# Kernel optimization log

Measured on AMD Instinct MI355X. Metric: run time of the kernel, lower is better.

The kernel has to match this reference:

```python
import jax, jax.numpy as jnp
import numpy as np

SINKHORN_ALPHA = 20.0
WEIGHT_LOSS_ECR = 100.0
OT_MAX_ITER = 100
STOP_THR = 0.005
EPS = 1e-16


def setup_inputs() -> dict:
    key = jax.random.key(0)
    # cost matrix: topics x vocab, nonnegative
    M = jax.random.uniform(key, (2000, 20000), dtype=jnp.float32)
    return {"M": M}


def reference(M):
    n, m = M.shape
    a = jnp.full((n, 1), 1.0 / n, dtype=M.dtype)  # uniform row marginal
    b = jnp.full((m, 1), 1.0 / m, dtype=M.dtype)  # uniform col marginal
    K = jnp.exp(-M * SINKHORN_ALPHA)              # Gibbs kernel, (n, m)

    u0 = jnp.full((n, 1), 1.0 / n, dtype=M.dtype)
    v0 = jnp.zeros((m, 1), dtype=M.dtype)
    err0 = jnp.asarray(1.0, dtype=M.dtype)
    cpt0 = jnp.asarray(0, dtype=jnp.int32)

    def cond(carry):
        u, v, err, cpt = carry
        return (err > STOP_THR) & (cpt < OT_MAX_ITER)

    def body(carry):
        u, v, err, cpt = carry
        v = b / (K.T @ u + EPS)          # (m, 1)
        u = a / (K @ v + EPS)            # (n, 1)
        cpt = cpt + 1
        # convergence check every 50 iterations (cpt % 50 == 1), as in torch
        bb = v * (K.T @ u)               # (m, 1) implied col marginal
        err_new = jnp.max(jnp.sum(jnp.abs(bb - b), axis=0))
        err = jnp.where(cpt % 50 == 1, err_new.astype(err.dtype), err)
        return (u, v, err, cpt)

    u, v, err, cpt = jax.lax.while_loop(cond, body, (u0, v0, err0, cpt0))

    transp = u * (K * v.T)               # transport plan, (n, m)
    loss_ECR = jnp.sum(transp * M)
    return loss_ECR * WEIGHT_LOSS_ECR
```

## Files before the change

### kernel.cpp

```cpp
#include <hip/hip_runtime.h>

typedef unsigned int uint32;
typedef unsigned long long uint64;
typedef float floatx2 __attribute__((ext_vector_type(2)));

#define ROWS_R 2000
#define COLS_R 20000
#define NBLK   256
#define NTHR   1024
#define NWAVE  16
#define CPB    80
#define CSTR   501
#define KDW    (CPB*CSTR)
#define KGUARD 16
#define USLOTS 101

static constexpr float A_MARG = 1.0f / 2000.0f;
static constexpr float B_MARG = 1.0f / 20000.0f;
static constexpr float EPSV   = 1e-16f;
static constexpr float THR    = 0.005f;
static constexpr float NALPHA = -20.0f;

__device__ __forceinline__ void st_dev_f32(float* p, float v) {
    __hip_atomic_store(p, v, __ATOMIC_RELAXED, __HIP_MEMORY_SCOPE_AGENT);
}
__device__ __forceinline__ float ld_dev_f32(const float* p) {
    return __hip_atomic_load(const_cast<float*>(p), __ATOMIC_RELAXED, __HIP_MEMORY_SCOPE_AGENT);
}
__device__ __forceinline__ void st_dev_f32x2(float* p, float x, float y) {
    union { float2 f; uint64 q; } u; u.f = make_float2(x, y);
    __hip_atomic_store(reinterpret_cast<uint64*>(p), u.q, __ATOMIC_RELAXED, __HIP_MEMORY_SCOPE_AGENT);
}
__device__ __forceinline__ float2 ld_dev_f32x2(const float* p) {
    union { float2 f; uint64 q; } u;
    u.q = __hip_atomic_load(reinterpret_cast<uint64*>(const_cast<float*>(p)),
                            __ATOMIC_RELAXED, __HIP_MEMORY_SCOPE_AGENT);
    return u.f;
}

__device__ __forceinline__ float halfpair_sum(float x) {
#if __has_builtin(__builtin_amdgcn_permlane32_swap)
    int xi = __float_as_int(x);
    auto sw = __builtin_amdgcn_permlane32_swap(xi, xi, false, false);
    return __int_as_float(sw[0]) + __int_as_float(sw[1]);
#else
    return x + __shfl_xor(x, 32, 64);
#endif
}

__device__ __forceinline__ void grid_barrier(uint32* ctrl, uint32 rnd) {
    asm volatile("s_waitcnt vmcnt(0)" ::: "memory");
    __syncthreads();
    if (threadIdx.x == 0) {
        const int gid = (int)(blockIdx.x >> 5);
        uint32* gcnt = ctrl + 128 + gid * 64;
        uint32* ggen = ctrl + 768 + gid * 64;
        uint32 a = __hip_atomic_fetch_add(gcnt, 1u, __ATOMIC_RELAXED, __HIP_MEMORY_SCOPE_AGENT);
        if (a == rnd * 32u + 31u) {
            uint32 r = __hip_atomic_fetch_add(ctrl, 1u, __ATOMIC_RELAXED, __HIP_MEMORY_SCOPE_AGENT);
            if (r == rnd * 8u + 7u) {
#pragma unroll
                for (int g = 0; g < 8; ++g)
                    __hip_atomic_store(ctrl + 768 + g * 64, rnd + 1u,
                                       __ATOMIC_RELAXED, __HIP_MEMORY_SCOPE_AGENT);
            }
        }
        while (__hip_atomic_load(ggen, __ATOMIC_RELAXED, __HIP_MEMORY_SCOPE_AGENT) < rnd + 1u)
            __builtin_amdgcn_s_sleep(1);
    }
    __syncthreads();
}

__global__ __launch_bounds__(256) void init_kernel(float* __restrict__ u_rot,
                                                   uint32* __restrict__ ctrl,
                                                   float* __restrict__ err2,
                                                   float* __restrict__ loss) {
    int idx = blockIdx.x * 256 + threadIdx.x;
    if (idx < 1280) ctrl[idx] = 0u;
    if (idx == 0) { err2[0] = 0.f; err2[1] = 0.f; *loss = 0.f; }
    if (idx < 2048) u_rot[idx] = (idx < ROWS_R) ? A_MARG : 0.0f;
}

__global__ __launch_bounds__(NTHR, 1) void sinkhorn_lds(
    const float* __restrict__ M,
    float* __restrict__ u_rot,
    float* __restrict__ P,
    uint32* __restrict__ ctrl,
    float* __restrict__ err2,
    float* __restrict__ loss,
    float* __restrict__ out) {
    __shared__ uint32 sK[KDW + KGUARD];
    __shared__ float  s_vloc[CPB];
    __shared__ float  s_vprev[CPB];
    __shared__ float  s_red[NWAVE * 8];
    __shared__ int    s_flag;

    const int tid  = threadIdx.x;
    const int lane = tid & 63;
    const int wav  = tid >> 6;
    const int b    = blockIdx.x;
    const int j0   = b * CPB;
    uint32 bar = 0;

    for (int i = tid; i < KDW + KGUARD; i += NTHR) sK[i] = 0u;
    __syncthreads();
    for (int q = wav; q < 500; q += NWAVE) {
#pragma unroll
        for (int ph = 0; ph < 2; ++ph) {
            const int cl = ph * 64 + lane;
            const int j  = j0 + cl;
            if ((ph == 0 || lane < 16) && j < COLS_R) {
                const float* mp = M + (size_t)(4 * q) * COLS_R + j;
                float k0 = __expf(NALPHA * mp[0]);
                float k1 = __expf(NALPHA * mp[COLS_R]);
                float k2 = __expf(NALPHA * mp[2 * COLS_R]);
                float k3 = __expf(NALPHA * mp[3 * COLS_R]);
                int lo = __builtin_amdgcn_cvt_pk_fp8_f32(k0, k1, 0, false);
                int hi = __builtin_amdgcn_cvt_pk_fp8_f32(k2, k3, lo, true);
                sK[cl * CSTR + q] = (uint32)hi;
            }
        }
    }
    __syncthreads();

    int usel = 0;

    for (int t = 1; t <= 100; ++t) {
        const bool chk  = (t == 2) || (t == 52);
        const int  slot = (t == 52) ? 1 : 0;

        const float4* u4 = reinterpret_cast<const float4*>(u_rot + (size_t)usel * 2048);
        float4 u_r[8];
#pragma unroll
        for (int s = 0; s < 8; ++s) u_r[s] = u4[s * 64 + lane];

        float e = 0.f;
#pragma unroll
        for (int q = 0; q < 5; ++q) {
            const int jl = wav * 5 + q;
            float acc = 0.f;
#pragma unroll
            for (int s = 0; s < 8; ++s) {
                uint32 kw = sK[jl * CSTR + s * 64 + lane];
                floatx2 f01 = __builtin_amdgcn_cvt_pk_f32_fp8(kw, false);
                floatx2 f23 = __builtin_amdgcn_cvt_pk_f32_fp8(kw, true);
                acc += f01.x * u_r[s].x + f01.y * u_r[s].y + f23.x * u_r[s].z + f23.y * u_r[s].w;
            }
            acc = halfpair_sum(acc);
#pragma unroll
            for (int o = 16; o; o >>= 1) acc += __shfl_xor(acc, o, 64);
            if (lane == 0) {
                float vnew = B_MARG / (acc + EPSV);
                if (chk) {
                    float vold = s_vloc[jl];
                    s_vprev[jl] = vold;
                    if (j0 + jl < COLS_R) e += fabsf(vold * acc - B_MARG);
                }
                s_vloc[jl] = vnew;
            }
        }
        if (chk && lane == 0) s_red[wav] = e;
        __syncthreads();

        float4 pa = make_float4(0.f, 0.f, 0.f, 0.f);
#pragma unroll 8
        for (int jp = 0; jp < 40; ++jp) {
            const int cl = 2 * jp + (lane >> 5);
            const int m  = lane & 31;
            uint32 kw = sK[cl * CSTR + wav * 32 + m];
            float  vv = s_vloc[cl];
            floatx2 f01 = __builtin_amdgcn_cvt_pk_f32_fp8(kw, false);
            floatx2 f23 = __builtin_amdgcn_cvt_pk_f32_fp8(kw, true);
            pa.x += f01.x * vv; pa.y += f01.y * vv;
            pa.z += f23.x * vv; pa.w += f23.y * vv;
        }
        pa.x = halfpair_sum(pa.x);
        pa.y = halfpair_sum(pa.y);
        pa.z = halfpair_sum(pa.z);
        pa.w = halfpair_sum(pa.w);
        if (lane < 32) {
            float* dst = P + (size_t)b * 2048 + wav * 128 + 4 * lane;
            st_dev_f32x2(dst,     pa.x, pa.y);
            st_dev_f32x2(dst + 2, pa.z, pa.w);
        }

        if (chk && tid == 0) {
            float s = 0.f;
            for (int k = 0; k < NWAVE; ++k) s += s_red[k];
            if (s != 0.f) atomicAdd(&err2[slot], s);
        }
        grid_barrier(ctrl, bar++);

        if (chk) {
            if (tid == 0) s_flag = (ld_dev_f32(&err2[slot]) <= THR) ? 1 : 0;
            __syncthreads();
            if (s_flag) {
                if (tid < CPB) s_vloc[tid] = s_vprev[tid];
                __syncthreads();
                break;
            }
        }

        {
            float v0 = ld_dev_f32(P + (size_t)(tid >> 3) * 2048 + 8 * b + (tid & 7));
            float v1 = ld_dev_f32(P + (size_t)((tid >> 3) + 128) * 2048 + 8 * b + (tid & 7));
            float s = v0 + v1;
            s += __shfl_xor(s, 8, 64);
            s += __shfl_xor(s, 16, 64);
            s = halfpair_sum(s);
            if (lane < 8) s_red[wav * 8 + lane] = s;
        }
        __syncthreads();
        if (tid < 8) {
            float s = 0.f;
            for (int w = 0; w < NWAVE; ++w) s += s_red[w * 8 + tid];
            const int row = 8 * b + tid;
            float val = (row < ROWS_R) ? A_MARG / (s + EPSV) : 0.0f;
            st_dev_f32(u_rot + (size_t)t * 2048 + row, val);
        }
        usel = t;
        grid_barrier(ctrl, bar++);
    }

    {
        const float* uf = u_rot + (size_t)usel * 2048;
        float acc = 0.f;
        for (int r = wav; r < ROWS_R; r += NWAVE) {
            const float uu = uf[r];
            const float* mp = M + (size_t)r * COLS_R + j0;
#pragma unroll
            for (int ph = 0; ph < 2; ++ph) {
                const int cl = ph * 64 + lane;
                if ((ph == 0 || lane < 16) && (j0 + cl) < COLS_R) {
                    float m = mp[cl];
                    acc += uu * __expf(NALPHA * m) * s_vloc[cl] * m;
                }
            }
        }
        acc = halfpair_sum(acc);
#pragma unroll
        for (int o = 16; o; o >>= 1) acc += __shfl_xor(acc, o, 64);
        if (lane == 0) s_red[wav] = acc;
        __syncthreads();
        if (tid == 0) {
            float s = 0.f;
            for (int k = 0; k < NWAVE; ++k) s += s_red[k];
            if (s != 0.f) atomicAdd(loss, s);
        }
    }
    grid_barrier(ctrl, bar++);
    if (b == 0 && tid == 0) out[0] = ld_dev_f32(loss) * 100.0f;
}


__device__ __forceinline__ float block_reduce_sum256(float v) {
#pragma unroll
    for (int o = 32; o; o >>= 1) v += __shfl_down(v, o, 64);
    __shared__ float smem[4];
    int lane = threadIdx.x & 63, w = threadIdx.x >> 6;
    if (lane == 0) smem[w] = v;
    __syncthreads();
    v = (threadIdx.x < 4) ? smem[threadIdx.x] : 0.0f;
    v += __shfl_down(v, 2, 64);
    v += __shfl_down(v, 1, 64);
    return v;
}

__global__ __launch_bounds__(256) void fb_init(float* u, float* vden, int* done, float* err, float* loss) {
    int idx = blockIdx.x * 256 + threadIdx.x;
    if (idx == 0) { *done = 0; *err = 0.0f; *loss = 0.0f; }
    if (idx < ROWS_R) u[idx] = A_MARG;
    if (idx < COLS_R) vden[idx] = 0.0f;
}
__global__ __launch_bounds__(256) void fb_colpass(const float* __restrict__ M, const float* __restrict__ u,
                                                  float* __restrict__ vden, const int* __restrict__ done) {
    if (*done) return;
    int c4 = blockIdx.x * 256 + threadIdx.x;
    if (c4 >= 5000) return;
    int r0 = blockIdx.y * 50;
    float4 acc = make_float4(0.f, 0.f, 0.f, 0.f);
    for (int r = r0; r < r0 + 50; ++r) {
        float ui = u[r];
        float4 mm = reinterpret_cast<const float4*>(M)[(size_t)r * 5000 + c4];
        acc.x += __expf(NALPHA * mm.x) * ui; acc.y += __expf(NALPHA * mm.y) * ui;
        acc.z += __expf(NALPHA * mm.z) * ui; acc.w += __expf(NALPHA * mm.w) * ui;
    }
    atomicAdd(&vden[c4 * 4 + 0], acc.x); atomicAdd(&vden[c4 * 4 + 1], acc.y);
    atomicAdd(&vden[c4 * 4 + 2], acc.z); atomicAdd(&vden[c4 * 4 + 3], acc.w);
}
__global__ __launch_bounds__(256) void fb_finv(float* v, float* vden, const int* done) {
    if (*done) return;
    int j = blockIdx.x * 256 + threadIdx.x;
    if (j < COLS_R) { v[j] = B_MARG / (vden[j] + EPSV); vden[j] = 0.0f; }
}
__global__ __launch_bounds__(256) void fb_rowpass(const float* __restrict__ M, const float* __restrict__ v,
                                                  float* __restrict__ u, const int* __restrict__ done) {
    if (*done) return;
    int row = blockIdx.x;
    const float4* v4 = reinterpret_cast<const float4*>(v);
    float acc = 0.0f;
    for (int c4 = threadIdx.x; c4 < 5000; c4 += 256) {
        float4 mm = reinterpret_cast<const float4*>(M)[(size_t)row * 5000 + c4];
        float4 vv = v4[c4];
        acc += __expf(NALPHA * mm.x) * vv.x + __expf(NALPHA * mm.y) * vv.y
             + __expf(NALPHA * mm.z) * vv.z + __expf(NALPHA * mm.w) * vv.w;
    }
    float s = block_reduce_sum256(acc);
    if (threadIdx.x == 0) u[row] = A_MARG / (s + EPSV);
}
__global__ __launch_bounds__(256) void fb_errfin(const float* v, float* vden, float* err, const int* done) {
    if (*done) return;
    int j = blockIdx.x * 256 + threadIdx.x;
    float local = 0.0f;
    if (j < COLS_R) { local = fabsf(v[j] * vden[j] - B_MARG); vden[j] = 0.0f; }
    float s = block_reduce_sum256(local);
    if (threadIdx.x == 0) atomicAdd(err, s);
}
__global__ void fb_check(int* done, float* err) {
    if (threadIdx.x == 0) { if (!*done && *err <= THR) *done = 1; *err = 0.0f; }
}
__global__ __launch_bounds__(256) void fb_loss(const float* __restrict__ M, const float* __restrict__ u,
                                               const float* __restrict__ v, float* __restrict__ loss) {
    int row = blockIdx.x;
    const float4* M4p = reinterpret_cast<const float4*>(M + (size_t)row * COLS_R);
    const float4* v4 = reinterpret_cast<const float4*>(v);
    float acc = 0.0f;
    for (int c4 = threadIdx.x; c4 < 5000; c4 += 256) {
        float4 mm = M4p[c4]; float4 vv = v4[c4];
        acc += __expf(NALPHA * mm.x) * vv.x * mm.x + __expf(NALPHA * mm.y) * vv.y * mm.y
             + __expf(NALPHA * mm.z) * vv.z * mm.z + __expf(NALPHA * mm.w) * vv.w * mm.w;
    }
    float s = block_reduce_sum256(acc);
    if (threadIdx.x == 0) atomicAdd(loss, s * u[row]);
}
__global__ void fb_writeout(float* out, const float* loss) {
    if (threadIdx.x == 0) out[0] = *loss * 100.0f;
}


extern "C" void kernel_launch(void* const* d_in, const int* in_sizes, int n_in,
                              void* d_out, int out_size, void* d_ws, size_t ws_size,
                              hipStream_t stream) {
    const float* M = (const float*)d_in[0];
    char* base = (char*)d_ws;

    const size_t OFF_CTRL = 0;
    const size_t OFF_ERR  = 8192;
    const size_t OFF_LOSS = 8320;
    const size_t OFF_UROT = 8448;
    const size_t OFF_P    = OFF_UROT + (size_t)USLOTS * 2048 * 4;
    const size_t NEED     = OFF_P + (size_t)NBLK * 2048 * 4;

    if (ws_size >= NEED) {
        uint32* ctrl  = (uint32*)(base + OFF_CTRL);
        float*  err2  = (float*)(base + OFF_ERR);
        float*  loss  = (float*)(base + OFF_LOSS);
        float*  u_rot = (float*)(base + OFF_UROT);
        float*  P     = (float*)(base + OFF_P);

        init_kernel<<<8, 256, 0, stream>>>(u_rot, ctrl, err2, loss);
        sinkhorn_lds<<<NBLK, NTHR, 0, stream>>>(M, u_rot, P, ctrl, err2, loss, (float*)d_out);
    } else {
        int*   done = (int*)(base + 0);
        float* err  = (float*)(base + 8);
        float* loss = (float*)(base + 16);
        float* u    = (float*)(base + 64);
        float* v    = (float*)(base + 64 + 8192);
        float* vden = (float*)(base + 64 + 8192 + 80000);

        fb_init<<<79, 256, 0, stream>>>(u, vden, done, err, loss);
        dim3 cgrid(20, 40);
        for (int t = 1; t <= 100; ++t) {
            fb_colpass<<<cgrid, 256, 0, stream>>>(M, u, vden, done);
            fb_finv<<<79, 256, 0, stream>>>(v, vden, done);
            fb_rowpass<<<ROWS_R, 256, 0, stream>>>(M, v, u, done);
            if (t == 1 || t == 51) {
                fb_colpass<<<cgrid, 256, 0, stream>>>(M, u, vden, done);
                fb_errfin<<<79, 256, 0, stream>>>(v, vden, err, done);
                fb_check<<<1, 64, 0, stream>>>(done, err);
            }
        }
        fb_loss<<<ROWS_R, 256, 0, stream>>>(M, u, v, loss);
        fb_writeout<<<1, 64, 0, stream>>>((float*)d_out, loss);
    }
}
```

Baseline: 329.2 us.

## Transpose partial-sum buffer so row reduction reads contiguous vectorized data

The K@v partial products are now written transposed: each block stores 8 consecutive rows per destination block slot, and each lane handles two packed K words (8 rows) over 4 column groups. The cross-block reduction then reads a contiguous 2048-float slab with float2 loads and reduces it with shuffles, replacing the earlier strided gather from 256 separate rows. This is meant to cut the latency and scattered traffic of the global exchange between grid barriers. In exchange it uses more registers per lane, and the partial stores are now scattered across blocks.

```diff
diff --git a/kernel.cpp b/kernel.cpp
--- a/kernel.cpp
+++ b/kernel.cpp
@@ -84,7 +84,7 @@
 __global__ __launch_bounds__(NTHR, 1) void sinkhorn_lds(
     const float* __restrict__ M,
     float* __restrict__ u_rot,
-    float* __restrict__ P,
+    float* __restrict__ P2,
     uint32* __restrict__ ctrl,
     float* __restrict__ err2,
     float* __restrict__ loss,
@@ -162,26 +162,42 @@
         if (chk && lane == 0) s_red[wav] = e;
         __syncthreads();
 
-        float4 pa = make_float4(0.f, 0.f, 0.f, 0.f);
-#pragma unroll 8
-        for (int jp = 0; jp < 40; ++jp) {
-            const int cl = 2 * jp + (lane >> 5);
-            const int m  = lane & 31;
-            uint32 kw = sK[cl * CSTR + wav * 32 + m];
-            float  vv = s_vloc[cl];
-            floatx2 f01 = __builtin_amdgcn_cvt_pk_f32_fp8(kw, false);
-            floatx2 f23 = __builtin_amdgcn_cvt_pk_f32_fp8(kw, true);
-            pa.x += f01.x * vv; pa.y += f01.y * vv;
-            pa.z += f23.x * vv; pa.w += f23.y * vv;
-        }
-        pa.x = halfpair_sum(pa.x);
-        pa.y = halfpair_sum(pa.y);
-        pa.z = halfpair_sum(pa.z);
-        pa.w = halfpair_sum(pa.w);
-        if (lane < 32) {
-            float* dst = P + (size_t)b * 2048 + wav * 128 + 4 * lane;
-            st_dev_f32x2(dst,     pa.x, pa.y);
-            st_dev_f32x2(dst + 2, pa.z, pa.w);
+        {
+            const int rg = lane >> 4;
+            const int rm = lane & 15;
+            const int qb = wav * 32 + 2 * rm;
+            float4 pb0 = make_float4(0.f, 0.f, 0.f, 0.f);
+            float4 pb1 = make_float4(0.f, 0.f, 0.f, 0.f);
+#pragma unroll 5
+            for (int jp = 0; jp < 20; ++jp) {
+                const int cl = jp * 4 + rg;
+                uint32 ka = sK[cl * CSTR + qb];
+                uint32 kb = sK[cl * CSTR + qb + 1];
+                float  vv = s_vloc[cl];
+                floatx2 a01 = __builtin_amdgcn_cvt_pk_f32_fp8(ka, false);
+                floatx2 a23 = __builtin_amdgcn_cvt_pk_f32_fp8(ka, true);
+                floatx2 b01 = __builtin_amdgcn_cvt_pk_f32_fp8(kb, false);
+                floatx2 b23 = __builtin_amdgcn_cvt_pk_f32_fp8(kb, true);
+                pb0.x += a01.x * vv; pb0.y += a01.y * vv;
+                pb0.z += a23.x * vv; pb0.w += a23.y * vv;
+                pb1.x += b01.x * vv; pb1.y += b01.y * vv;
+                pb1.z += b23.x * vv; pb1.w += b23.y * vv;
+            }
+            pb0.x += __shfl_xor(pb0.x, 16, 64);  pb0.y += __shfl_xor(pb0.y, 16, 64);
+            pb0.z += __shfl_xor(pb0.z, 16, 64);  pb0.w += __shfl_xor(pb0.w, 16, 64);
+            pb1.x += __shfl_xor(pb1.x, 16, 64);  pb1.y += __shfl_xor(pb1.y, 16, 64);
+            pb1.z += __shfl_xor(pb1.z, 16, 64);  pb1.w += __shfl_xor(pb1.w, 16, 64);
+            pb0.x = halfpair_sum(pb0.x);  pb0.y = halfpair_sum(pb0.y);
+            pb0.z = halfpair_sum(pb0.z);  pb0.w = halfpair_sum(pb0.w);
+            pb1.x = halfpair_sum(pb1.x);  pb1.y = halfpair_sum(pb1.y);
+            pb1.z = halfpair_sum(pb1.z);  pb1.w = halfpair_sum(pb1.w);
+            if (lane < 16) {
+                float* dst = P2 + (size_t)(wav * 16 + lane) * 2048 + b * 8;
+                st_dev_f32x2(dst,     pb0.x, pb0.y);
+                st_dev_f32x2(dst + 2, pb0.z, pb0.w);
+                st_dev_f32x2(dst + 4, pb1.x, pb1.y);
+                st_dev_f32x2(dst + 6, pb1.z, pb1.w);
+            }
         }
 
         if (chk && tid == 0) {
@@ -202,13 +218,15 @@
         }
 
         {
-            float v0 = ld_dev_f32(P + (size_t)(tid >> 3) * 2048 + 8 * b + (tid & 7));
-            float v1 = ld_dev_f32(P + (size_t)((tid >> 3) + 128) * 2048 + 8 * b + (tid & 7));
-            float s = v0 + v1;
-            s += __shfl_xor(s, 8, 64);
-            s += __shfl_xor(s, 16, 64);
-            s = halfpair_sum(s);
-            if (lane < 8) s_red[wav * 8 + lane] = s;
+            float2 pr = ld_dev_f32x2(P2 + (size_t)b * 2048 + tid * 2);
+            pr.x += __shfl_xor(pr.x, 4, 64);   pr.y += __shfl_xor(pr.y, 4, 64);
+            pr.x += __shfl_xor(pr.x, 8, 64);   pr.y += __shfl_xor(pr.y, 8, 64);
+            pr.x += __shfl_xor(pr.x, 16, 64);  pr.y += __shfl_xor(pr.y, 16, 64);
+            pr.x = halfpair_sum(pr.x);         pr.y = halfpair_sum(pr.y);
+            if (lane < 4) {
+                s_red[wav * 8 + 2 * lane]     = pr.x;
+                s_red[wav * 8 + 2 * lane + 1] = pr.y;
+            }
         }
         __syncthreads();
         if (tid < 8) {
@@ -356,10 +374,10 @@
         float*  err2  = (float*)(base + OFF_ERR);
         float*  loss  = (float*)(base + OFF_LOSS);
         float*  u_rot = (float*)(base + OFF_UROT);
-        float*  P     = (float*)(base + OFF_P);
+        float*  P2    = (float*)(base + OFF_P);
 
         init_kernel<<<8, 256, 0, stream>>>(u_rot, ctrl, err2, loss);
-        sinkhorn_lds<<<NBLK, NTHR, 0, stream>>>(M, u_rot, P, ctrl, err2, loss, (float*)d_out);
+        sinkhorn_lds<<<NBLK, NTHR, 0, stream>>>(M, u_rot, P2, ctrl, err2, loss, (float*)d_out);
     } else {
         int*   done = (int*)(base + 0);
         float* err  = (float*)(base + 8);
```

Result: no change. 335.1 us (+1.8%).
